# Kernel tuning notes

Measured on AMD Instinct MI355X. Metric: run time of the kernel, lower is better.

## Reference

```python
import jax, jax.numpy as jnp
import numpy as np

N_USERS = 30000
N_ENT = 70000
N = N_USERS + N_ENT          # total graph nodes
E = 1_600_000                # edges (avg degree 16)
D = 64                       # embed_dim
B = 4096                     # scored user-item pairs
LEAKY_SLOPE = 0.01           # torch nn.LeakyReLU default
EPS = 1e-12                  # torch F.normalize default eps


def setup_inputs() -> dict:
    key = jax.random.key(0)
    ks = jax.random.split(key, 16)
    inp = {
        "edge_row": jax.random.randint(ks[0], (E,), 0, N, dtype=jnp.int32),
        "edge_col": jax.random.randint(ks[1], (E,), 0, N, dtype=jnp.int32),
        "edge_vals": jax.random.uniform(ks[2], (E,), dtype=jnp.float32) / 16.0,
        "user_embed": jax.random.normal(ks[3], (N_USERS, D), jnp.float32) * 0.1,
        "entity_embed": jax.random.normal(ks[4], (N_ENT, D), jnp.float32) * 0.1,
        "W1_0": jax.random.normal(ks[5], (D, 64), jnp.float32) * (1.0 / np.sqrt(D)),
        "b1_0": jnp.zeros((64,), jnp.float32),
        "W2_0": jax.random.normal(ks[6], (D, 64), jnp.float32) * (1.0 / np.sqrt(D)),
        "b2_0": jnp.zeros((64,), jnp.float32),
        "W1_1": jax.random.normal(ks[7], (64, 32), jnp.float32) * (1.0 / 8.0),
        "b1_1": jnp.zeros((32,), jnp.float32),
        "W2_1": jax.random.normal(ks[8], (64, 32), jnp.float32) * (1.0 / 8.0),
        "b2_1": jnp.zeros((32,), jnp.float32),
        "user_ids": jax.random.randint(ks[9], (B,), 0, N_USERS, dtype=jnp.int32),
        "item_ids": jax.random.randint(ks[10], (B,), 0, N_ENT, dtype=jnp.int32),
    }
    return inp


def _gnn_layer(feats, edge_row, edge_col, edge_vals, W1, b1, W2, b2):
    # sparse adj @ feats  ==  scatter-add of weighted source features to rows
    gathered = feats[edge_col] * edge_vals[:, None]          # (E, d_in)
    h_neigh = jax.ops.segment_sum(gathered, edge_row, num_segments=N)  # (N, d_in)
    term1 = (feats + h_neigh) @ W1 + b1
    term2 = (feats * h_neigh) @ W2 + b2
    h = jax.nn.leaky_relu(term1 + term2, negative_slope=LEAKY_SLOPE)
    # F.normalize(h, p=2, dim=1)
    norm = jnp.linalg.norm(h, axis=1, keepdims=True)
    return h / jnp.maximum(norm, EPS)


def reference(edge_row, edge_col, edge_vals, user_embed, entity_embed,
              W1_0, b1_0, W2_0, b2_0, W1_1, b1_1, W2_1, b2_1,
              user_ids, item_ids):
    a0 = jnp.concatenate([user_embed, entity_embed], axis=0)     # (N, 64)
    a1 = _gnn_layer(a0, edge_row, edge_col, edge_vals, W1_0, b1_0, W2_0, b2_0)  # (N, 64)
    a2 = _gnn_layer(a1, edge_row, edge_col, edge_vals, W1_1, b1_1, W2_1, b2_1)  # (N, 32)
    final = jnp.concatenate([a0, a1, a2], axis=1)                # (N, 160)
    u = final[user_ids]                                          # (B, 160)
    i = final[N_USERS + item_ids]                                # (B, 160)
    return jnp.sum(u * i, axis=1)                                # (B,)
```

## Files before the change

### kernel.cpp

```cpp
#include <hip/hip_runtime.h>
#include <hip/hip_bf16.h>
#include <math.h>

#define LEAKY 0.01f
#define SCAN_BLOCK 256
#define SCAN_ITEMS 4
#define SCAN_TILE (SCAN_BLOCK * SCAN_ITEMS)

__global__ void zero_i32(int* __restrict__ p, int n) {
    int i = blockIdx.x * blockDim.x + threadIdx.x;
    if (i < n) p[i] = 0;
}

__global__ void count_edges(const int* __restrict__ row, int E,
                            int* __restrict__ deg, int* __restrict__ rank) {
    int i = blockIdx.x * blockDim.x + threadIdx.x;
    if (i < E) rank[i] = atomicAdd(&deg[row[i]], 1);
}

__global__ __launch_bounds__(SCAN_BLOCK) void scan_phase1(
    const int* __restrict__ deg, int* __restrict__ blocksum, int N) {
    __shared__ int red[SCAN_BLOCK];
    int b = blockIdx.x, t = threadIdx.x;
    int base = b * SCAN_TILE + t * SCAN_ITEMS;
    int s = 0;
#pragma unroll
    for (int j = 0; j < SCAN_ITEMS; j++) {
        int i = base + j;
        if (i < N) s += deg[i];
    }
    red[t] = s;
    __syncthreads();
    for (int off = SCAN_BLOCK / 2; off > 0; off >>= 1) {
        if (t < off) red[t] += red[t + off];
        __syncthreads();
    }
    if (t == 0) blocksum[b] = red[0];
}

__global__ __launch_bounds__(1024) void scan_phase2(
    const int* __restrict__ blocksum, int* __restrict__ blockoff,
    int* __restrict__ row_ptr, int G, int N) {
    __shared__ int sums[1024];
    int t = threadIdx.x;
    sums[t] = (t < G) ? blocksum[t] : 0;
    __syncthreads();
    for (int off = 1; off < 1024; off <<= 1) {
        int v = (t >= off) ? sums[t - off] : 0;
        __syncthreads();
        sums[t] += v;
        __syncthreads();
    }
    if (t < G) blockoff[t] = (t == 0) ? 0 : sums[t - 1];
    if (t == G - 1) row_ptr[N] = sums[t];
}

__global__ __launch_bounds__(SCAN_BLOCK) void scan_phase3(
    const int* __restrict__ deg, const int* __restrict__ blockoff,
    int* __restrict__ row_ptr, int N) {
    __shared__ int red[SCAN_BLOCK];
    int b = blockIdx.x, t = threadIdx.x;
    int base = b * SCAN_TILE + t * SCAN_ITEMS;
    int v[SCAN_ITEMS];
    int s = 0;
#pragma unroll
    for (int j = 0; j < SCAN_ITEMS; j++) {
        int i = base + j;
        v[j] = (i < N) ? deg[i] : 0;
        s += v[j];
    }
    red[t] = s;
    __syncthreads();
    for (int off = 1; off < SCAN_BLOCK; off <<= 1) {
        int x = (t >= off) ? red[t - off] : 0;
        __syncthreads();
        red[t] += x;
        __syncthreads();
    }
    int run = blockoff[b] + ((t == 0) ? 0 : red[t - 1]);
#pragma unroll
    for (int j = 0; j < SCAN_ITEMS; j++) {
        int i = base + j;
        if (i < N) { row_ptr[i] = run; run += v[j]; }
    }
}

__global__ void build_a0(const float4* __restrict__ ue, const float4* __restrict__ ee,
                         float4* __restrict__ a0, int nu4, int ntot4) {
    int i = blockIdx.x * blockDim.x + threadIdx.x;
    if (i < ntot4) a0[i] = (i < nu4) ? ue[i] : ee[i - nu4];
}

__global__ void fill_csr(const int* __restrict__ row, const int* __restrict__ col,
                         const float* __restrict__ val, const int* __restrict__ rank,
                         const int* __restrict__ row_ptr, int E,
                         int2* __restrict__ csr) {
    int i = blockIdx.x * blockDim.x + threadIdx.x;
    if (i < E) {
        int p = row_ptr[row[i]] + rank[i];
        csr[p] = make_int2(col[i], __float_as_int(val[i]));
    }
}

__device__ __forceinline__ void fma4(float o[4], float sv, const float4& wv) {
    o[0] = fmaf(sv, wv.x, o[0]);
    o[1] = fmaf(sv, wv.y, o[1]);
    o[2] = fmaf(sv, wv.z, o[2]);
    o[3] = fmaf(sv, wv.w, o[3]);
}

template<int DOUT>
__global__ __launch_bounds__(256, 4) void gnn_layer(
    const float* __restrict__ feats, const int2* __restrict__ csr,
    const int* __restrict__ row_ptr,
    const float* __restrict__ W1, const float* __restrict__ b1,
    const float* __restrict__ W2, const float* __restrict__ b2,
    float* __restrict__ out, int N) {
    __shared__ __align__(16) float S[32 * 132];
    int wv = threadIdx.x >> 6, lane = threadIdx.x & 63;
    int nb = blockIdx.x * 32 + wv * 8;

    for (int ni = 0; ni < 8; ni++) {
        int node = nb + ni;
        if (node >= N) break;
        float x = feats[node * 64 + lane];
        int e0 = row_ptr[node], e1 = row_ptr[node + 1];
        float acc = 0.f;
        int e = e0;
        for (; e + 4 <= e1; e += 4) {
            int2 p0 = csr[e], p1 = csr[e + 1], p2 = csr[e + 2], p3 = csr[e + 3];
            float f0 = feats[p0.x * 64 + lane];
            float f1 = feats[p1.x * 64 + lane];
            float f2 = feats[p2.x * 64 + lane];
            float f3 = feats[p3.x * 64 + lane];
            acc = fmaf(__int_as_float(p0.y), f0, acc);
            acc = fmaf(__int_as_float(p1.y), f1, acc);
            acc = fmaf(__int_as_float(p2.y), f2, acc);
            acc = fmaf(__int_as_float(p3.y), f3, acc);
        }
        for (; e < e1; e++) {
            int2 p = csr[e];
            acc = fmaf(__int_as_float(p.y), feats[p.x * 64 + lane], acc);
        }
        float* sp = &S[(wv * 8 + ni) * 132];
        sp[lane]      = x + acc;
        sp[64 + lane] = x * acc;
    }
    __threadfence_block();

    if constexpr (DOUT == 64) {
        int strip = lane & 15, g = lane >> 4;
        int d0 = strip * 4;
        float4 b1v = *(const float4*)&b1[d0];
        float4 b2v = *(const float4*)&b2[d0];
        float oa[4] = {b1v.x + b2v.x, b1v.y + b2v.y, b1v.z + b2v.z, b1v.w + b2v.w};
        float ob[4] = {oa[0], oa[1], oa[2], oa[3]};
        const float* spa = &S[(wv * 8 + 2 * g) * 132];
        const float* spb = spa + 132;
#pragma unroll
        for (int half = 0; half < 2; half++) {
            const float* W  = half ? W2 : W1;
            const float* sa = spa + half * 64;
            const float* sb = spb + half * 64;
#pragma unroll 2
            for (int k = 0; k < 64; k += 4) {
                float4 va = *(const float4*)&sa[k];
                float4 vb = *(const float4*)&sb[k];
                float4 wr0 = *(const float4*)&W[(k + 0) * 64 + d0];
                float4 wr1 = *(const float4*)&W[(k + 1) * 64 + d0];
                float4 wr2 = *(const float4*)&W[(k + 2) * 64 + d0];
                float4 wr3 = *(const float4*)&W[(k + 3) * 64 + d0];
                fma4(oa, va.x, wr0); fma4(oa, va.y, wr1);
                fma4(oa, va.z, wr2); fma4(oa, va.w, wr3);
                fma4(ob, vb.x, wr0); fma4(ob, vb.y, wr1);
                fma4(ob, vb.z, wr2); fma4(ob, vb.w, wr3);
            }
        }
#pragma unroll
        for (int t = 0; t < 2; t++) {
            float* o = t ? ob : oa;
            float h0 = (o[0] > 0.f) ? o[0] : LEAKY * o[0];
            float h1 = (o[1] > 0.f) ? o[1] : LEAKY * o[1];
            float h2 = (o[2] > 0.f) ? o[2] : LEAKY * o[2];
            float h3 = (o[3] > 0.f) ? o[3] : LEAKY * o[3];
            float ss = h0 * h0 + h1 * h1 + h2 * h2 + h3 * h3;
            ss += __shfl_xor(ss, 1, 64);
            ss += __shfl_xor(ss, 2, 64);
            ss += __shfl_xor(ss, 4, 64);
            ss += __shfl_xor(ss, 8, 64);
            float sc = 1.0f / fmaxf(sqrtf(ss), 1e-12f);
            int node = nb + 2 * g + t;
            if (node < N) {
                float4 r = {h0 * sc, h1 * sc, h2 * sc, h3 * sc};
                *(float4*)&out[node * 64 + d0] = r;
            }
        }
    } else {
        int strip = lane & 7, nI = lane >> 3;
        int d0 = strip * 4;
        float4 b1v = *(const float4*)&b1[d0];
        float4 b2v = *(const float4*)&b2[d0];
        float o[4] = {b1v.x + b2v.x, b1v.y + b2v.y, b1v.z + b2v.z, b1v.w + b2v.w};
        const float* sp = &S[(wv * 8 + nI) * 132];
#pragma unroll
        for (int half = 0; half < 2; half++) {
            const float* W  = half ? W2 : W1;
            const float* sv = sp + half * 64;
#pragma unroll 2
            for (int k = 0; k < 64; k += 4) {
                float4 v   = *(const float4*)&sv[k];
                float4 wr0 = *(const float4*)&W[(k + 0) * 32 + d0];
                float4 wr1 = *(const float4*)&W[(k + 1) * 32 + d0];
                float4 wr2 = *(const float4*)&W[(k + 2) * 32 + d0];
                float4 wr3 = *(const float4*)&W[(k + 3) * 32 + d0];
                fma4(o, v.x, wr0); fma4(o, v.y, wr1);
                fma4(o, v.z, wr2); fma4(o, v.w, wr3);
            }
        }
        float h0 = (o[0] > 0.f) ? o[0] : LEAKY * o[0];
        float h1 = (o[1] > 0.f) ? o[1] : LEAKY * o[1];
        float h2 = (o[2] > 0.f) ? o[2] : LEAKY * o[2];
        float h3 = (o[3] > 0.f) ? o[3] : LEAKY * o[3];
        float ss = h0 * h0 + h1 * h1 + h2 * h2 + h3 * h3;
        ss += __shfl_xor(ss, 1, 64);
        ss += __shfl_xor(ss, 2, 64);
        ss += __shfl_xor(ss, 4, 64);
        float sc = 1.0f / fmaxf(sqrtf(ss), 1e-12f);
        int node = nb + nI;
        if (node < N) {
            float4 r = {h0 * sc, h1 * sc, h2 * sc, h3 * sc};
            *(float4*)&out[node * 32 + d0] = r;
        }
    }
}

__global__ __launch_bounds__(256) void score_pairs(
    const float* __restrict__ a0, const float* __restrict__ a1,
    const float* __restrict__ a2,
    const int* __restrict__ uid, const int* __restrict__ iid,
    float* __restrict__ out, int B, int NU) {
    int wave = threadIdx.x >> 6, lane = threadIdx.x & 63;
    int p = blockIdx.x * 4 + wave;
    if (p >= B) return;
    int u = uid[p], it = iid[p];
    size_t un = (size_t)u, in = (size_t)(NU + it);
    float s = a0[un * 64 + lane] * a0[in * 64 + lane];
    s = fmaf(a1[un * 64 + lane], a1[in * 64 + lane], s);
    if (lane < 32) s = fmaf(a2[un * 32 + lane], a2[in * 32 + lane], s);
#pragma unroll
    for (int m = 32; m >= 1; m >>= 1) s += __shfl_xor(s, m, 64);
    if (lane == 0) out[p] = s;
}

extern "C" void kernel_launch(void* const* d_in, const int* in_sizes, int n_in,
                              void* d_out, int out_size, void* d_ws, size_t ws_size,
                              hipStream_t stream) {
    const int*   edge_row  = (const int*)d_in[0];
    const int*   edge_col  = (const int*)d_in[1];
    const float* edge_vals = (const float*)d_in[2];
    const float* ue        = (const float*)d_in[3];
    const float* ee        = (const float*)d_in[4];
    const float* W1_0 = (const float*)d_in[5];
    const float* b1_0 = (const float*)d_in[6];
    const float* W2_0 = (const float*)d_in[7];
    const float* b2_0 = (const float*)d_in[8];
    const float* W1_1 = (const float*)d_in[9];
    const float* b1_1 = (const float*)d_in[10];
    const float* W2_1 = (const float*)d_in[11];
    const float* b2_1 = (const float*)d_in[12];
    const int*   uid  = (const int*)d_in[13];
    const int*   iid  = (const int*)d_in[14];
    float* out = (float*)d_out;

    const int E  = in_sizes[0];
    const int NU = in_sizes[3] / 64;
    const int NE = in_sizes[4] / 64;
    const int N  = NU + NE;
    const int B  = in_sizes[13];
    const int G  = (N + SCAN_TILE - 1) / SCAN_TILE;

    char* ws = (char*)d_ws;
    size_t off = 0;
    auto alloc = [&](size_t bytes) -> char* {
        char* p = ws + off;
        off = (off + bytes + 255) & ~(size_t)255;
        return p;
    };
    int*   deg      = (int*)alloc((size_t)N * 4);
    int*   rank     = (int*)alloc((size_t)E * 4);
    int*   row_ptr  = (int*)alloc((size_t)(N + 1) * 4);
    int*   blocksum = (int*)alloc((size_t)1024 * 4);
    int*   blockoff = (int*)alloc((size_t)1024 * 4);
    int2*  csr      = (int2*)alloc((size_t)E * 8);
    float* a0       = (float*)alloc((size_t)N * 64 * 4);
    float* a1       = (float*)alloc((size_t)N * 64 * 4);
    float* a2       = (float*)alloc((size_t)N * 32 * 4);
    (void)ws_size; (void)n_in; (void)out_size; (void)NE;

    zero_i32<<<(N + 255) / 256, 256, 0, stream>>>(deg, N);
    count_edges<<<(E + 255) / 256, 256, 0, stream>>>(edge_row, E, deg, rank);
    scan_phase1<<<G, SCAN_BLOCK, 0, stream>>>(deg, blocksum, N);
    scan_phase2<<<1, 1024, 0, stream>>>(blocksum, blockoff, row_ptr, G, N);
    scan_phase3<<<G, SCAN_BLOCK, 0, stream>>>(deg, blockoff, row_ptr, N);
    fill_csr<<<(E + 255) / 256, 256, 0, stream>>>(edge_row, edge_col, edge_vals,
                                                  rank, row_ptr, E, csr);
    int ntot4 = N * 16, nu4 = NU * 16;
    build_a0<<<(ntot4 + 255) / 256, 256, 0, stream>>>((const float4*)ue, (const float4*)ee,
                                                      (float4*)a0, nu4, ntot4);
    gnn_layer<64><<<(N + 31) / 32, 256, 0, stream>>>(a0, csr, row_ptr,
                                                     W1_0, b1_0, W2_0, b2_0, a1, N);
    gnn_layer<32><<<(N + 31) / 32, 256, 0, stream>>>(a1, csr, row_ptr,
                                                     W1_1, b1_1, W2_1, b2_1, a2, N);
    score_pairs<<<(B + 3) / 4, 256, 0, stream>>>(a0, a1, a2, uid, iid, out, B, NU);
}
```

Before: 455.7 us.

## Gather neighbor features from bf16 copies with wave-cooperative CSR loading

Writes bf16 shadow copies of a0 and a1 alongside the fp32 tensors and gathers neighbor features from those copies during aggregation, halving the bytes read by the random gather. CSR entries are now loaded cooperatively, one per lane, and broadcast with shuffles in chunks of eight, replacing per-lane redundant loads. The trade-off is reduced precision in the aggregated neighbor sums, plus extra bf16 writes and workspace.

```diff
diff --git a/kernel.cpp b/kernel.cpp
--- a/kernel.cpp
+++ b/kernel.cpp
@@ -6,6 +6,8 @@
 #define SCAN_BLOCK 256
 #define SCAN_ITEMS 4
 #define SCAN_TILE (SCAN_BLOCK * SCAN_ITEMS)
+
+struct __align__(8) Bf4 { __hip_bfloat16 a, b, c, d; };
 
 __global__ void zero_i32(int* __restrict__ p, int n) {
     int i = blockIdx.x * blockDim.x + threadIdx.x;
@@ -86,9 +88,16 @@
 }
 
 __global__ void build_a0(const float4* __restrict__ ue, const float4* __restrict__ ee,
-                         float4* __restrict__ a0, int nu4, int ntot4) {
+                         float4* __restrict__ a0, __hip_bfloat16* __restrict__ a0b,
+                         int nu4, int ntot4) {
     int i = blockIdx.x * blockDim.x + threadIdx.x;
-    if (i < ntot4) a0[i] = (i < nu4) ? ue[i] : ee[i - nu4];
+    if (i < ntot4) {
+        float4 v = (i < nu4) ? ue[i] : ee[i - nu4];
+        a0[i] = v;
+        Bf4 q = {__float2bfloat16(v.x), __float2bfloat16(v.y),
+                 __float2bfloat16(v.z), __float2bfloat16(v.w)};
+        *(Bf4*)&a0b[(size_t)i * 4] = q;
+    }
 }
 
 __global__ void fill_csr(const int* __restrict__ row, const int* __restrict__ col,
@@ -111,11 +120,11 @@
 
 template<int DOUT>
 __global__ __launch_bounds__(256, 4) void gnn_layer(
-    const float* __restrict__ feats, const int2* __restrict__ csr,
-    const int* __restrict__ row_ptr,
+    const float* __restrict__ feats, const __hip_bfloat16* __restrict__ featsb,
+    const int2* __restrict__ csr, const int* __restrict__ row_ptr,
     const float* __restrict__ W1, const float* __restrict__ b1,
     const float* __restrict__ W2, const float* __restrict__ b2,
-    float* __restrict__ out, int N) {
+    float* __restrict__ out, __hip_bfloat16* __restrict__ outb, int N) {
     __shared__ __align__(16) float S[32 * 132];
     int wv = threadIdx.x >> 6, lane = threadIdx.x & 63;
     int nb = blockIdx.x * 32 + wv * 8;
@@ -123,24 +132,29 @@
     for (int ni = 0; ni < 8; ni++) {
         int node = nb + ni;
         if (node >= N) break;
-        float x = feats[node * 64 + lane];
-        int e0 = row_ptr[node], e1 = row_ptr[node + 1];
+        float x = feats[(size_t)node * 64 + lane];
+        int e0 = row_ptr[node];
+        int degn = row_ptr[node + 1] - e0;
         float acc = 0.f;
-        int e = e0;
-        for (; e + 4 <= e1; e += 4) {
-            int2 p0 = csr[e], p1 = csr[e + 1], p2 = csr[e + 2], p3 = csr[e + 3];
-            float f0 = feats[p0.x * 64 + lane];
-            float f1 = feats[p1.x * 64 + lane];
-            float f2 = feats[p2.x * 64 + lane];
-            float f3 = feats[p3.x * 64 + lane];
-            acc = fmaf(__int_as_float(p0.y), f0, acc);
-            acc = fmaf(__int_as_float(p1.y), f1, acc);
-            acc = fmaf(__int_as_float(p2.y), f2, acc);
-            acc = fmaf(__int_as_float(p3.y), f3, acc);
-        }
-        for (; e < e1; e++) {
-            int2 p = csr[e];
-            acc = fmaf(__int_as_float(p.y), feats[p.x * 64 + lane], acc);
+        int done = 0;
+        while (done < degn) {
+            int take = min(64, degn - done);
+            int2 m = make_int2(0, 0);
+            if (lane < take) m = csr[e0 + done + lane];
+            int nch = (take + 7) >> 3;
+            for (int c2 = 0; c2 < nch; c2++) {
+                int base = c2 * 8;
+                float fv[8], vv[8];
+#pragma unroll
+                for (int u = 0; u < 8; u++) {
+                    int col = __shfl(m.x, base + u, 64);
+                    vv[u] = __int_as_float(__shfl(m.y, base + u, 64));
+                    fv[u] = __bfloat162float(featsb[(size_t)col * 64 + lane]);
+                }
+#pragma unroll
+                for (int u = 0; u < 8; u++) acc = fmaf(vv[u], fv[u], acc);
+            }
+            done += take;
         }
         float* sp = &S[(wv * 8 + ni) * 132];
         sp[lane]      = x + acc;
@@ -192,7 +206,10 @@
             int node = nb + 2 * g + t;
             if (node < N) {
                 float4 r = {h0 * sc, h1 * sc, h2 * sc, h3 * sc};
-                *(float4*)&out[node * 64 + d0] = r;
+                *(float4*)&out[(size_t)node * 64 + d0] = r;
+                Bf4 q = {__float2bfloat16(r.x), __float2bfloat16(r.y),
+                         __float2bfloat16(r.z), __float2bfloat16(r.w)};
+                *(Bf4*)&outb[(size_t)node * 64 + d0] = q;
             }
         }
     } else {
@@ -229,7 +246,7 @@
         int node = nb + nI;
         if (node < N) {
             float4 r = {h0 * sc, h1 * sc, h2 * sc, h3 * sc};
-            *(float4*)&out[node * 32 + d0] = r;
+            *(float4*)&out[(size_t)node * 32 + d0] = r;
         }
     }
 }
@@ -295,6 +312,8 @@
     float* a0       = (float*)alloc((size_t)N * 64 * 4);
     float* a1       = (float*)alloc((size_t)N * 64 * 4);
     float* a2       = (float*)alloc((size_t)N * 32 * 4);
+    __hip_bfloat16* a0b = (__hip_bfloat16*)alloc((size_t)N * 64 * 2);
+    __hip_bfloat16* a1b = (__hip_bfloat16*)alloc((size_t)N * 64 * 2);
     (void)ws_size; (void)n_in; (void)out_size; (void)NE;
 
     zero_i32<<<(N + 255) / 256, 256, 0, stream>>>(deg, N);
@@ -306,10 +325,10 @@
                                                   rank, row_ptr, E, csr);
     int ntot4 = N * 16, nu4 = NU * 16;
     build_a0<<<(ntot4 + 255) / 256, 256, 0, stream>>>((const float4*)ue, (const float4*)ee,
-                                                      (float4*)a0, nu4, ntot4);
-    gnn_layer<64><<<(N + 31) / 32, 256, 0, stream>>>(a0, csr, row_ptr,
-                                                     W1_0, b1_0, W2_0, b2_0, a1, N);
-    gnn_layer<32><<<(N + 31) / 32, 256, 0, stream>>>(a1, csr, row_ptr,
-                                                     W1_1, b1_1, W2_1, b2_1, a2, N);
+                                                      (float4*)a0, a0b, nu4, ntot4);
+    gnn_layer<64><<<(N + 31) / 32, 256, 0, stream>>>(a0, a0b, csr, row_ptr,
+                                                     W1_0, b1_0, W2_0, b2_0, a1, a1b, N);
+    gnn_layer<32><<<(N + 31) / 32, 256, 0, stream>>>(a1, a1b, csr, row_ptr,
+                                                     W1_1, b1_1, W2_1, b2_1, a2, nullptr, N);
     score_pairs<<<(B + 3) / 4, 256, 0, stream>>>(a0, a1, a2, uid, iid, out, B, NU);
 }
```

New measurement: 398.1 us. 1.14x faster.
